# Kernel optimization log

Hardware: AMD Instinct MI355X
Metric: run time of the kernel (lower is better)

Reference implementation:

```python
import jax, jax.numpy as jnp
import numpy as np

B, SQ, SKV, DIN = 2, 2048, 2048, 2048
Q_HEADS, KV_HEADS, DIMS = 16, 4, 2048
HEAD_DIM = DIMS // Q_HEADS  # 128
REP = Q_HEADS // KV_HEADS   # 4


def setup_inputs() -> dict:
    key = jax.random.key(0)
    ks = jax.random.split(key, 6)
    scale = lambda fan_in: 1.0 / np.sqrt(fan_in)
    return {
        "q": jax.random.normal(ks[0], (B, SQ, DIN), jnp.float32),
        "kv": jax.random.normal(ks[1], (B, SKV, DIN), jnp.float32),
        "mask": jnp.ones((1, 1, SQ, SKV), jnp.float32),
        "Wq": jax.random.normal(ks[2], (DIN, Q_HEADS * HEAD_DIM), jnp.float32) * scale(DIN),
        "Wk": jax.random.normal(ks[3], (DIN, KV_HEADS * HEAD_DIM), jnp.float32) * scale(DIN),
        "Wv": jax.random.normal(ks[4], (DIN, KV_HEADS * HEAD_DIM), jnp.float32) * scale(DIN),
        "Wo": jax.random.normal(ks[5], (Q_HEADS * HEAD_DIM, DIN), jnp.float32) * scale(Q_HEADS * HEAD_DIM),
    }


def reference(q, kv, mask, Wq, Wk, Wv, Wo):
    b, sq, _ = q.shape
    skv = kv.shape[1]
    xq = q @ Wq                      # [b, sq, q_heads*head_dim]
    xk = kv @ Wk                     # [b, skv, kv_heads*head_dim]
    xv = kv @ Wv
    # faithful to source: element-wise repeat along feature axis, THEN head reshape
    xk = jnp.repeat(xk, REP, axis=-1)
    xv = jnp.repeat(xv, REP, axis=-1)
    xq = xq.reshape(b, sq, Q_HEADS, HEAD_DIM).transpose(0, 2, 1, 3)   # [b,h,sq,d]
    xk = xk.reshape(b, skv, Q_HEADS, HEAD_DIM).transpose(0, 2, 1, 3)  # [b,h,skv,d]
    xv = xv.reshape(b, skv, Q_HEADS, HEAD_DIM).transpose(0, 2, 1, 3)
    scores = jnp.einsum("bhqd,bhkd->bhqk", xq, xk) * (HEAD_DIM ** -0.5)
    scores = scores - (1.0 / mask - 1.0)
    attn = jax.nn.softmax(scores, axis=-1)
    out = jnp.einsum("bhqk,bhkd->bhqd", attn, xv)
    out = out.transpose(0, 2, 1, 3).reshape(b, sq, Q_HEADS * HEAD_DIM)
    return out @ Wo
```

## Files before the change

### kernel.cpp

```cpp
#include <hip/hip_runtime.h>
#include <hip/hip_bf16.h>
#include <stdint.h>

typedef short short8 __attribute__((ext_vector_type(8)));
typedef short short4v __attribute__((ext_vector_type(4)));
typedef float floatx4 __attribute__((ext_vector_type(4)));

#define AS1 __attribute__((address_space(1)))
#define AS3 __attribute__((address_space(3)))
#define DEV static __device__ __forceinline__

#if __has_builtin(__builtin_amdgcn_mfma_f32_16x16x16bf16_1k)
#define HAVE_MFMA16 1
#else
#define HAVE_MFMA16 0
#endif

DEV uint16_t f2bf(float x) {
  union { float f; uint32_t u; } v; v.f = x;
  return (uint16_t)((v.u + 0x7fffu + ((v.u >> 16) & 1u)) >> 16);
}

DEV uint32_t cvtpk(float a, float b) {
  uint32_t r;
  asm("v_cvt_pk_bf16_f32 %0, %1, %2" : "=v"(r) : "v"(a), "v"(b));
  return r;
}


DEV void cvt_bf16_f(const float* __restrict__ src, uint16_t* __restrict__ dst, int bid) {
  int i = bid * 256 + threadIdx.x;
  float4 v = ((const float4*)src)[i];
  union { uint16_t u[4]; uint64_t q; } o;
  o.u[0] = f2bf(v.x); o.u[1] = f2bf(v.y); o.u[2] = f2bf(v.z); o.u[3] = f2bf(v.w);
  ((uint64_t*)dst)[i] = o.q;
}

DEV void mask_scan_f(const float* __restrict__ mask, uint32_t* __restrict__ f, int bid) {
  int i = bid * 256 + threadIdx.x;
  const float4* p = (const float4*)mask;
  float4 a = p[i * 2], b = p[i * 2 + 1];
  bool bad = (a.x != 1.f) | (a.y != 1.f) | (a.z != 1.f) | (a.w != 1.f) |
             (b.x != 1.f) | (b.y != 1.f) | (b.z != 1.f) | (b.w != 1.f);
  if (bad) *f = 0u;
}

DEV void fold_wq_f(float (*tile)[33], const float* __restrict__ Wq,
                   uint16_t* __restrict__ WqFT, int bid) {
  const int t = threadIdx.x;
  const int j0 = (bid / 64) * 32, k0 = (bid % 64) * 32;
  {
    const int tj = t & 31, tk8 = t >> 5;
    const int j = j0 + tj;
    const int base = 128 * (j >> 5) + 4 * (j & 31);
    for (int kk = 0; kk < 4; ++kk) {
      int kl = tk8 * 4 + kk;
      float4 w = *(const float4*)(Wq + (size_t)(k0 + kl) * 2048 + base);
      tile[tj][kl] = w.x + w.y + w.z + w.w;
    }
  }
  __syncthreads();
  {
    const int tk = t & 31, tj8 = t >> 5;
    for (int jj = 0; jj < 4; ++jj) {
      int jl = tj8 * 4 + jj;
      WqFT[(size_t)(j0 + jl) * 2048 + k0 + tk] = f2bf(tile[jl][tk]);
    }
  }
}

DEV void wkv_t_f(float (*tile)[33], const float* __restrict__ Wk,
                 const float* __restrict__ Wv, uint16_t* __restrict__ WkvT, int bid) {
  const int t = threadIdx.x;
  const int j0 = (bid / 64) * 32, k0 = (bid % 64) * 32;
  const float* src = (j0 < 512) ? Wk : Wv;
  const int jb = (j0 < 512) ? j0 : j0 - 512;
  {
    const int tj = t & 31, tk8 = t >> 5;
    for (int kk = 0; kk < 4; ++kk) {
      int kl = tk8 * 4 + kk;
      tile[tj][kl] = src[(size_t)(k0 + kl) * 512 + jb + tj];
    }
  }
  __syncthreads();
  {
    const int tk = t & 31, tj8 = t >> 5;
    for (int jj = 0; jj < 4; ++jj) {
      int jl = tj8 * 4 + jj;
      WkvT[(size_t)(j0 + jl) * 2048 + k0 + tk] = f2bf(tile[jl][tk]);
    }
  }
}

DEV void wof_t_f(float (*tile)[33], const float* __restrict__ Wo,
                 uint16_t* __restrict__ WoFT, int bid) {
  const int t = threadIdx.x;
  const int n0 = (bid / 16) * 32, j0 = (bid % 16) * 32;
  {
    const int tn = t & 31, tj8 = t >> 5;
    for (int jj = 0; jj < 4; ++jj) {
      int jl = tj8 * 4 + jj;
      int j = j0 + jl;
      int base = 128 * (j >> 5) + 4 * (j & 31);
      float ssum = 0.f;
      for (int r = 0; r < 4; ++r) ssum += Wo[(size_t)(base + r) * 2048 + n0 + tn];
      tile[tn][jl] = ssum;
    }
  }
  __syncthreads();
  {
    const int tj = t & 31, tn8 = t >> 5;
    for (int nn = 0; nn < 4; ++nn) {
      int nl = tn8 * 4 + nn;
      WoFT[(size_t)(n0 + nl) * 512 + j0 + tj] = f2bf(tile[nl][tj]);
    }
  }
}

__global__ __launch_bounds__(256) void prep_k(const float* __restrict__ q,
                                              const float* __restrict__ kv,
                                              const float* __restrict__ mask,
                                              const float* __restrict__ Wq,
                                              const float* __restrict__ Wk,
                                              const float* __restrict__ Wv,
                                              const float* __restrict__ Wo,
                                              uint16_t* __restrict__ qb,
                                              uint16_t* __restrict__ kvb,
                                              uint16_t* __restrict__ WqFT,
                                              uint16_t* __restrict__ WkvT,
                                              uint16_t* __restrict__ WoFT,
                                              uint32_t* __restrict__ flag) {
  __shared__ float tile[32][33];
  const int bid = blockIdx.x;
  if (bid < 8192)        cvt_bf16_f(q, qb, bid);
  else if (bid < 16384)  cvt_bf16_f(kv, kvb, bid - 8192);
  else if (bid < 18432)  mask_scan_f(mask, flag, bid - 16384);
  else if (bid < 19456)  fold_wq_f(tile, Wq, WqFT, bid - 18432);
  else if (bid < 21504)  wkv_t_f(tile, Wk, Wv, WkvT, bid - 19456);
  else                   wof_t_f(tile, Wo, WoFT, bid - 21504);
}

template <typename OutT, int BM, int BN, int FA, int FB>
DEV void gemm_dev(uint16_t* __restrict__ As, uint16_t* __restrict__ Bs,
                  const uint16_t* __restrict__ A, const uint16_t* __restrict__ BT,
                  OutT* __restrict__ C, int N, int K, float scale, int m0, int n0) {
  constexpr int BK = 64;
  const int lane = threadIdx.x & 63, wave = threadIdx.x >> 6;
  const int lo = lane & 15, g = lane >> 4;
  const int wm = wave >> 1, wn = wave & 1;
  constexpr int CA = BM / 32, CB = BN / 32;
  floatx4 acc[FA][FB] = {};

  for (int k0 = 0; k0 < K; k0 += BK) {
#pragma unroll
    for (int c = 0; c < CA; ++c) {
      int slot = (wave * CA + c) * 64 + lane;
      int row = slot >> 3, col = (slot & 7) * 8;
      __builtin_amdgcn_global_load_lds((const AS1 uint32_t*)(A + (size_t)(m0 + row) * K + k0 + col),
                                       (AS3 uint32_t*)(As + (size_t)(wave * CA + c) * 512), 16, 0, 0);
    }
#pragma unroll
    for (int c = 0; c < CB; ++c) {
      int slot = (wave * CB + c) * 64 + lane;
      int row = slot >> 3, col = (slot & 7) * 8;
      __builtin_amdgcn_global_load_lds((const AS1 uint32_t*)(BT + (size_t)(n0 + row) * K + k0 + col),
                                       (AS3 uint32_t*)(Bs + (size_t)(wave * CB + c) * 512), 16, 0, 0);
    }
    __syncthreads();
#pragma unroll
    for (int kk = 0; kk < BK; kk += 32) {
      short8 af[FA], bf[FB];
#pragma unroll
      for (int fa = 0; fa < FA; ++fa)
        af[fa] = *(const short8*)&As[(wm * FA * 16 + fa * 16 + lo) * BK + kk + g * 8];
#pragma unroll
      for (int fb = 0; fb < FB; ++fb)
        bf[fb] = *(const short8*)&Bs[(wn * FB * 16 + fb * 16 + lo) * BK + kk + g * 8];
#pragma unroll
      for (int fa = 0; fa < FA; ++fa)
#pragma unroll
        for (int fb = 0; fb < FB; ++fb)
          acc[fa][fb] = __builtin_amdgcn_mfma_f32_16x16x32_bf16(af[fa], bf[fb], acc[fa][fb], 0, 0, 0);
    }
    __syncthreads();
  }
#pragma unroll
  for (int fa = 0; fa < FA; ++fa)
#pragma unroll
    for (int fb = 0; fb < FB; ++fb)
#pragma unroll
      for (int r = 0; r < 4; ++r) {
        int row = m0 + wm * FA * 16 + fa * 16 + g * 4 + r;
        int col = n0 + wn * FB * 16 + fb * 16 + lo;
        if constexpr (sizeof(OutT) == 2)
          C[(size_t)row * N + col] = (OutT)f2bf(acc[fa][fb][r] * scale);
        else
          C[(size_t)row * N + col] = (OutT)(acc[fa][fb][r] * scale);
      }
}

__global__ __launch_bounds__(256) void proj_k(const uint16_t* __restrict__ qb,
                                              const uint16_t* __restrict__ kvb,
                                              const uint16_t* __restrict__ WqFT,
                                              const uint16_t* __restrict__ WkvT,
                                              uint16_t* __restrict__ Qf,
                                              uint16_t* __restrict__ XK,
                                              uint16_t* __restrict__ VT,
                                              float scale2) {
  __shared__ __attribute__((aligned(16))) uint16_t As[128 * 64];
  __shared__ __attribute__((aligned(16))) uint16_t Bs[64 * 64];
  const int bid = blockIdx.x;
  const int lb = (bid & 7) * 96 + (bid >> 3);
  if (lb < 256) {
    gemm_dev<uint16_t, 128, 64, 4, 2>(As, Bs, qb, WqFT, Qf, 512, 2048, scale2,
                                      (lb >> 3) * 128, (lb & 7) * 64);
  } else if (lb < 512) {
    const int t = lb - 256;
    gemm_dev<uint16_t, 128, 64, 4, 2>(As, Bs, kvb, WkvT, XK, 512, 2048, 1.0f,
                                      (t >> 3) * 128, (t & 7) * 64);
  } else {
    const int t = lb - 512;
    const int b = t >> 7, r = t & 127;
    gemm_dev<uint16_t, 128, 64, 4, 2>(As, Bs, WkvT + 512 * 2048,
                                      kvb + (size_t)b * 2048 * 2048,
                                      VT + (size_t)b * 512 * 2048,
                                      2048, 2048, 1.0f, (r & 3) * 128, (r >> 2) * 64);
  }
}

__global__ __launch_bounds__(256) void oproj_k(const uint16_t* __restrict__ A,
                                               const uint16_t* __restrict__ BT,
                                               float* __restrict__ C) {
  __shared__ __attribute__((aligned(16))) uint16_t As[128 * 64];
  __shared__ __attribute__((aligned(16))) uint16_t Bs[64 * 64];
  const int lb = (blockIdx.x & 7) * 128 + (blockIdx.x >> 3);
  gemm_dev<float, 128, 64, 4, 2>(As, Bs, A, BT, C, 2048, 512, 1.0f,
                                 (lb >> 5) * 128, (lb & 31) * 64);
}

__global__ __launch_bounds__(256) void attn_k(const uint16_t* __restrict__ Qf,
                                              const uint16_t* __restrict__ XK,
                                              const uint16_t* __restrict__ VT,
                                              const float* __restrict__ mask,
                                              const uint32_t* __restrict__ flag,
                                              float* __restrict__ Pacc,
                                              float2* __restrict__ Pms) {
  __shared__ __attribute__((aligned(16))) uint16_t Ks[2][64 * 32];
  __shared__ __attribute__((aligned(16))) uint16_t Vs[2][32 * 64];
  const int tid = threadIdx.x;
  const int lane = tid & 63, w = tid >> 6;
  const int lo = lane & 15, g = lane >> 4;
  const int bid = blockIdx.x;
  const int lb = (bid & 7) * 256 + (bid >> 3);
  const int qt = lb & 31, h = (lb >> 5) & 15, b = (lb >> 9) & 1, half = lb >> 10;
  const int q0 = qt * 64 + w * 16;
  const int kvbase = half * 1024;
  const bool trivial = (*flag != 0u);
  const float LOG2E = 1.4426950408889634f;

  short8 qf = *(const short8*)(Qf + ((size_t)(b * 2048 + q0 + lo)) * 512 + h * 32 + g * 8);

  const int sK = w * 64 + lane;
  const int rK = sK >> 2;
  const int cKg = (sK & 3) ^ (rK & 3) ^ ((rK >> 2) & 3);
  const uint16_t* Ksrc = XK + ((size_t)(b * 2048 + kvbase + rK)) * 512 + h * 32 + cKg * 8;
  const int fV = sK >> 3, cV = ((sK & 7) - fV) & 7;
  const uint16_t* Vsrc = VT + ((size_t)(b * 512 + h * 32 + fV)) * 2048 + kvbase + cV * 8;

  const int swzL = (lo & 3) ^ ((lo >> 2) & 3);
  const int cK = (g ^ swzL) * 8;
#if !HAVE_MFMA16
  const int vA = (((g) + lo) & 7) * 8;
  const int vB = (((g + 4) + lo) & 7) * 8;
  const int srcA = lo + 16 * ((2 * g) & 3);
  const int srcB = lo + 16 * ((2 * g + 1) & 3);
#endif

  float m = -1e30f, sp = 0.f;
  floatx4 acc0 = {0.f, 0.f, 0.f, 0.f}, acc1 = {0.f, 0.f, 0.f, 0.f};
  const floatx4 zf = {0.f, 0.f, 0.f, 0.f};

  __builtin_amdgcn_global_load_lds((const AS1 uint32_t*)Ksrc,
                                   (AS3 uint32_t*)(&Ks[0][0] + w * 512), 16, 0, 0);
  __builtin_amdgcn_global_load_lds((const AS1 uint32_t*)Vsrc,
                                   (AS3 uint32_t*)(&Vs[0][0] + w * 512), 16, 0, 0);
  asm volatile("s_waitcnt vmcnt(0)" ::: "memory");
  __syncthreads();

  int buf = 0;
  for (int t = 0; t < 16; ++t) {
    if (t < 15) {
      __builtin_amdgcn_global_load_lds((const AS1 uint32_t*)(Ksrc + (size_t)(t + 1) * 64 * 512),
                                       (AS3 uint32_t*)(&Ks[buf ^ 1][0] + w * 512), 16, 0, 0);
      __builtin_amdgcn_global_load_lds((const AS1 uint32_t*)(Vsrc + (size_t)(t + 1) * 64),
                                       (AS3 uint32_t*)(&Vs[buf ^ 1][0] + w * 512), 16, 0, 0);
    }
    const uint16_t* Kb = &Ks[buf][0];
    const uint16_t* Vb = &Vs[buf][0];
    const int k0 = kvbase + t * 64;

    short8 kf0 = *(const short8*)(Kb + (lo) * 32 + cK);
    short8 kf1 = *(const short8*)(Kb + (lo + 16) * 32 + cK);
    short8 kf2 = *(const short8*)(Kb + (lo + 32) * 32 + cK);
    short8 kf3 = *(const short8*)(Kb + (lo + 48) * 32 + cK);
    floatx4 s0 = __builtin_amdgcn_mfma_f32_16x16x32_bf16(kf0, qf, zf, 0, 0, 0);
    floatx4 s1 = __builtin_amdgcn_mfma_f32_16x16x32_bf16(kf1, qf, zf, 0, 0, 0);
    floatx4 s2 = __builtin_amdgcn_mfma_f32_16x16x32_bf16(kf2, qf, zf, 0, 0, 0);
    floatx4 s3 = __builtin_amdgcn_mfma_f32_16x16x32_bf16(kf3, qf, zf, 0, 0, 0);

    if (!trivial) {
      const float* mp = mask + (size_t)(q0 + lo) * 2048 + k0 + g * 4;
      float4 m0v = *(const float4*)(mp);
      float4 m1v = *(const float4*)(mp + 16);
      float4 m2v = *(const float4*)(mp + 32);
      float4 m3v = *(const float4*)(mp + 48);
      s0[0] -= (1.f / m0v.x - 1.f) * LOG2E; s0[1] -= (1.f / m0v.y - 1.f) * LOG2E;
      s0[2] -= (1.f / m0v.z - 1.f) * LOG2E; s0[3] -= (1.f / m0v.w - 1.f) * LOG2E;
      s1[0] -= (1.f / m1v.x - 1.f) * LOG2E; s1[1] -= (1.f / m1v.y - 1.f) * LOG2E;
      s1[2] -= (1.f / m1v.z - 1.f) * LOG2E; s1[3] -= (1.f / m1v.w - 1.f) * LOG2E;
      s2[0] -= (1.f / m2v.x - 1.f) * LOG2E; s2[1] -= (1.f / m2v.y - 1.f) * LOG2E;
      s2[2] -= (1.f / m2v.z - 1.f) * LOG2E; s2[3] -= (1.f / m2v.w - 1.f) * LOG2E;
      s3[0] -= (1.f / m3v.x - 1.f) * LOG2E; s3[1] -= (1.f / m3v.y - 1.f) * LOG2E;
      s3[2] -= (1.f / m3v.z - 1.f) * LOG2E; s3[3] -= (1.f / m3v.w - 1.f) * LOG2E;
    }

    float t0 = fmaxf(fmaxf(s0[0], s0[1]), s0[2]);
    float t1 = fmaxf(fmaxf(s0[3], s1[0]), s1[1]);
    float t2 = fmaxf(fmaxf(s1[2], s1[3]), s2[0]);
    float t3 = fmaxf(fmaxf(s2[1], s2[2]), s2[3]);
    float t4 = fmaxf(fmaxf(s3[0], s3[1]), s3[2]);
    float pmax = fmaxf(fmaxf(fmaxf(t0, t1), t2), fmaxf(fmaxf(t3, t4), s3[3]));

    if (!__all(pmax - m <= 8.f)) {
      float tm = fmaxf(pmax, __shfl_xor(pmax, 16));
      tm = fmaxf(tm, __shfl_xor(tm, 32));
      float mn = fmaxf(m, tm);
      float f = __builtin_amdgcn_exp2f(m - mn);
      sp *= f;
#pragma unroll
      for (int r = 0; r < 4; ++r) { acc0[r] *= f; acc1[r] *= f; }
      m = mn;
    }

    float p0[4], p1[4], p2[4], p3[4];
#pragma unroll
    for (int r = 0; r < 4; ++r) {
      p0[r] = __builtin_amdgcn_exp2f(s0[r] - m);
      p1[r] = __builtin_amdgcn_exp2f(s1[r] - m);
      p2[r] = __builtin_amdgcn_exp2f(s2[r] - m);
      p3[r] = __builtin_amdgcn_exp2f(s3[r] - m);
    }
    sp += ((p0[0] + p0[1]) + (p0[2] + p0[3])) + ((p1[0] + p1[1]) + (p1[2] + p1[3])) +
          ((p2[0] + p2[1]) + (p2[2] + p2[3])) + ((p3[0] + p3[1]) + (p3[2] + p3[3]));

#if HAVE_MFMA16
#pragma unroll
    for (int c = 0; c < 4; ++c) {
      const float* pc = (c == 0) ? p0 : (c == 1) ? p1 : (c == 2) ? p2 : p3;
      union { uint32_t u[2]; short4v v; } pk;
      pk.u[0] = cvtpk(pc[0], pc[1]);
      pk.u[1] = cvtpk(pc[2], pc[3]);
      const int kc = 2 * c + (g >> 1);
      const int pA = (kc + lo) & 7;
      const int pB = (kc + lo + 16) & 7;
      short4v va = *(const short4v*)(Vb + lo * 64 + pA * 8 + (g & 1) * 4);
      short4v vb = *(const short4v*)(Vb + (lo + 16) * 64 + pB * 8 + (g & 1) * 4);
      acc0 = __builtin_amdgcn_mfma_f32_16x16x16bf16_1k(va, pk.v, acc0, 0, 0, 0);
      acc1 = __builtin_amdgcn_mfma_f32_16x16x16bf16_1k(vb, pk.v, acc1, 0, 0, 0);
    }
#else
    uint32_t u0 = cvtpk(p0[0], p0[1]), u1 = cvtpk(p0[2], p0[3]);
    uint32_t u2 = cvtpk(p1[0], p1[1]), u3 = cvtpk(p1[2], p1[3]);
    uint32_t u4 = cvtpk(p2[0], p2[1]), u5 = cvtpk(p2[2], p2[3]);
    uint32_t u6 = cvtpk(p3[0], p3[1]), u7 = cvtpk(p3[2], p3[3]);
    union { uint32_t u[4]; short8 v; } pfa, pfb;
    {
      uint32_t x0 = (uint32_t)__shfl((int)u0, srcA), x2 = (uint32_t)__shfl((int)u2, srcA);
      uint32_t x1 = (uint32_t)__shfl((int)u1, srcA), x3 = (uint32_t)__shfl((int)u3, srcA);
      uint32_t y0 = (uint32_t)__shfl((int)u0, srcB), y2 = (uint32_t)__shfl((int)u2, srcB);
      uint32_t y1 = (uint32_t)__shfl((int)u1, srcB), y3 = (uint32_t)__shfl((int)u3, srcB);
      pfa.u[0] = (g < 2) ? x0 : x2;
      pfa.u[1] = (g < 2) ? x1 : x3;
      pfa.u[2] = (g < 2) ? y0 : y2;
      pfa.u[3] = (g < 2) ? y1 : y3;
    }
    {
      uint32_t x4 = (uint32_t)__shfl((int)u4, srcA), x6 = (uint32_t)__shfl((int)u6, srcA);
      uint32_t x5 = (uint32_t)__shfl((int)u5, srcA), x7 = (uint32_t)__shfl((int)u7, srcA);
      uint32_t y4 = (uint32_t)__shfl((int)u4, srcB), y6 = (uint32_t)__shfl((int)u6, srcB);
      uint32_t y5 = (uint32_t)__shfl((int)u5, srcB), y7 = (uint32_t)__shfl((int)u7, srcB);
      pfb.u[0] = (g < 2) ? x4 : x6;
      pfb.u[1] = (g < 2) ? x5 : x7;
      pfb.u[2] = (g < 2) ? y4 : y6;
      pfb.u[3] = (g < 2) ? y5 : y7;
    }
    short8 v0a = *(const short8*)(Vb + lo * 64 + vA);
    short8 v1a = *(const short8*)(Vb + (lo + 16) * 64 + vA);
    short8 v0b = *(const short8*)(Vb + lo * 64 + vB);
    short8 v1b = *(const short8*)(Vb + (lo + 16) * 64 + vB);
    acc0 = __builtin_amdgcn_mfma_f32_16x16x32_bf16(v0a, pfa.v, acc0, 0, 0, 0);
    acc1 = __builtin_amdgcn_mfma_f32_16x16x32_bf16(v1a, pfa.v, acc1, 0, 0, 0);
    acc0 = __builtin_amdgcn_mfma_f32_16x16x32_bf16(v0b, pfb.v, acc0, 0, 0, 0);
    acc1 = __builtin_amdgcn_mfma_f32_16x16x32_bf16(v1b, pfb.v, acc1, 0, 0, 0);
#endif

    asm volatile("s_waitcnt vmcnt(0)" ::: "memory");
    __syncthreads();
    buf ^= 1;
  }
  float s = sp;
  s += __shfl_xor(s, 16);
  s += __shfl_xor(s, 32);

  const size_t qidx = ((size_t)((half * 2 + b) * 16 + h)) * 2048 + q0 + lo;
  float* pacc = Pacc + qidx * 32;
  *(floatx4*)(pacc + 4 * g) = acc0;
  *(floatx4*)(pacc + 16 + 4 * g) = acc1;
  if (g == 0) Pms[qidx] = make_float2(m, s);
}

__global__ __launch_bounds__(256) void combine_k(const float* __restrict__ Pacc,
                                                 const float2* __restrict__ Pms,
                                                 uint16_t* __restrict__ O32) {
  const int t = blockIdx.x * 256 + threadIdx.x;
  const int f4 = t & 7;
  const int qq = (t >> 3) & 2047;
  const int h = (t >> 14) & 15;
  const int b = t >> 18;
  const size_t qidx0 = ((size_t)((0 + b) * 16 + h)) * 2048 + qq;
  const size_t qidx1 = ((size_t)((2 + b) * 16 + h)) * 2048 + qq;
  float2 ms0 = Pms[qidx0], ms1 = Pms[qidx1];
  float M = fmaxf(ms0.x, ms1.x);
  float w0 = __builtin_amdgcn_exp2f(ms0.x - M);
  float w1 = __builtin_amdgcn_exp2f(ms1.x - M);
  float inv = 1.0f / (ms0.y * w0 + ms1.y * w1);
  w0 *= inv; w1 *= inv;
  float4 a0 = *(const float4*)(Pacc + qidx0 * 32 + f4 * 4);
  float4 a1 = *(const float4*)(Pacc + qidx1 * 32 + f4 * 4);
  union { uint16_t u[4]; uint64_t q; } o;
  o.u[0] = f2bf(a0.x * w0 + a1.x * w1);
  o.u[1] = f2bf(a0.y * w0 + a1.y * w1);
  o.u[2] = f2bf(a0.z * w0 + a1.z * w1);
  o.u[3] = f2bf(a0.w * w0 + a1.w * w1);
  *(uint64_t*)(O32 + ((size_t)(b * 2048 + qq)) * 512 + h * 32 + f4 * 4) = o.q;
}

extern "C" void kernel_launch(void* const* d_in, const int* in_sizes, int n_in,
                              void* d_out, int out_size, void* d_ws, size_t ws_size,
                              hipStream_t stream) {
  const float* q    = (const float*)d_in[0];
  const float* kv   = (const float*)d_in[1];
  const float* mask = (const float*)d_in[2];
  const float* Wq   = (const float*)d_in[3];
  const float* Wk   = (const float*)d_in[4];
  const float* Wv   = (const float*)d_in[5];
  const float* Wo   = (const float*)d_in[6];

  char* ws = (char*)d_ws;
  uint16_t* qb    = (uint16_t*)(ws);
  uint16_t* kvb   = (uint16_t*)(ws + (16ull << 20));
  uint16_t* Qf    = (uint16_t*)(ws + (32ull << 20));
  uint16_t* XK    = (uint16_t*)(ws + (36ull << 20));
  uint16_t* VT    = (uint16_t*)(ws + (40ull << 20));
  uint16_t* O32   = (uint16_t*)(ws + (48ull << 20));
  uint16_t* WqFT  = (uint16_t*)(ws + (52ull << 20));
  uint16_t* WkvT  = (uint16_t*)(ws + (54ull << 20));
  uint16_t* WoFT  = (uint16_t*)(ws + (58ull << 20));
  uint32_t* flag  = (uint32_t*)(ws + (60ull << 20));
  float*    Pacc  = (float*)(ws);
  float2*   Pms   = (float2*)(ws + (16ull << 20));

  const float SCALE2 = 0.08838834764831845f * 1.4426950408889634f;

  hipMemsetAsync(flag, 1, 4, stream);
  prep_k<<<22528, 256, 0, stream>>>(q, kv, mask, Wq, Wk, Wv, Wo,
                                    qb, kvb, WqFT, WkvT, WoFT, flag);
  proj_k<<<768, 256, 0, stream>>>(qb, kvb, WqFT, WkvT, Qf, XK, VT, SCALE2);
  attn_k<<<2048, 256, 0, stream>>>(Qf, XK, VT, mask, flag, Pacc, Pms);
  combine_k<<<2048, 256, 0, stream>>>(Pacc, Pms, O32);
  oproj_k<<<1024, 256, 0, stream>>>(O32, WoFT, (float*)d_out);
}
```

Before: 141.4 us.

## Double-buffer LDS tiles in GEMM to overlap global loads with MFMA

The shared GEMM routine now keeps two LDS buffers for A and B and issues the next K-tile's global-to-LDS loads before computing on the current tile. Each iteration then ends with one vmcnt wait and barrier instead of two barriers, so load latency can hide behind MFMA work in the projection and output-projection kernels. In exchange, LDS use per block doubles to 48 KB, which may lower occupancy.

```diff
diff --git a/kernel.cpp b/kernel.cpp
--- a/kernel.cpp
+++ b/kernel.cpp
@@ -151,38 +151,54 @@
   constexpr int CA = BM / 32, CB = BN / 32;
   floatx4 acc[FA][FB] = {};
 
-  for (int k0 = 0; k0 < K; k0 += BK) {
+  auto stage = [&](int bf, int kk0) {
 #pragma unroll
     for (int c = 0; c < CA; ++c) {
       int slot = (wave * CA + c) * 64 + lane;
       int row = slot >> 3, col = (slot & 7) * 8;
-      __builtin_amdgcn_global_load_lds((const AS1 uint32_t*)(A + (size_t)(m0 + row) * K + k0 + col),
-                                       (AS3 uint32_t*)(As + (size_t)(wave * CA + c) * 512), 16, 0, 0);
+      __builtin_amdgcn_global_load_lds(
+          (const AS1 uint32_t*)(A + (size_t)(m0 + row) * K + kk0 + col),
+          (AS3 uint32_t*)(As + (size_t)bf * BM * BK + (size_t)(wave * CA + c) * 512),
+          16, 0, 0);
     }
 #pragma unroll
     for (int c = 0; c < CB; ++c) {
       int slot = (wave * CB + c) * 64 + lane;
       int row = slot >> 3, col = (slot & 7) * 8;
-      __builtin_amdgcn_global_load_lds((const AS1 uint32_t*)(BT + (size_t)(n0 + row) * K + k0 + col),
-                                       (AS3 uint32_t*)(Bs + (size_t)(wave * CB + c) * 512), 16, 0, 0);
-    }
+      __builtin_amdgcn_global_load_lds(
+          (const AS1 uint32_t*)(BT + (size_t)(n0 + row) * K + kk0 + col),
+          (AS3 uint32_t*)(Bs + (size_t)bf * BN * BK + (size_t)(wave * CB + c) * 512),
+          16, 0, 0);
+    }
+  };
+
+  stage(0, 0);
+  asm volatile("s_waitcnt vmcnt(0)" ::: "memory");
+  __syncthreads();
+
+  int bf = 0;
+  for (int k0 = 0; k0 < K; k0 += BK) {
+    if (k0 + BK < K) stage(bf ^ 1, k0 + BK);
+    const uint16_t* Ab = As + (size_t)bf * BM * BK;
+    const uint16_t* Bb = Bs + (size_t)bf * BN * BK;
+#pragma unroll
+    for (int kk = 0; kk < BK; kk += 32) {
+      short8 af[FA], bfr[FB];
+#pragma unroll
+      for (int fa = 0; fa < FA; ++fa)
+        af[fa] = *(const short8*)&Ab[(wm * FA * 16 + fa * 16 + lo) * BK + kk + g * 8];
+#pragma unroll
+      for (int fb = 0; fb < FB; ++fb)
+        bfr[fb] = *(const short8*)&Bb[(wn * FB * 16 + fb * 16 + lo) * BK + kk + g * 8];
+#pragma unroll
+      for (int fa = 0; fa < FA; ++fa)
+#pragma unroll
+        for (int fb = 0; fb < FB; ++fb)
+          acc[fa][fb] = __builtin_amdgcn_mfma_f32_16x16x32_bf16(af[fa], bfr[fb], acc[fa][fb], 0, 0, 0);
+    }
+    asm volatile("s_waitcnt vmcnt(0)" ::: "memory");
     __syncthreads();
-#pragma unroll
-    for (int kk = 0; kk < BK; kk += 32) {
-      short8 af[FA], bf[FB];
-#pragma unroll
-      for (int fa = 0; fa < FA; ++fa)
-        af[fa] = *(const short8*)&As[(wm * FA * 16 + fa * 16 + lo) * BK + kk + g * 8];
-#pragma unroll
-      for (int fb = 0; fb < FB; ++fb)
-        bf[fb] = *(const short8*)&Bs[(wn * FB * 16 + fb * 16 + lo) * BK + kk + g * 8];
-#pragma unroll
-      for (int fa = 0; fa < FA; ++fa)
-#pragma unroll
-        for (int fb = 0; fb < FB; ++fb)
-          acc[fa][fb] = __builtin_amdgcn_mfma_f32_16x16x32_bf16(af[fa], bf[fb], acc[fa][fb], 0, 0, 0);
-    }
-    __syncthreads();
+    bf ^= 1;
   }
 #pragma unroll
   for (int fa = 0; fa < FA; ++fa)
@@ -207,8 +223,8 @@
                                               uint16_t* __restrict__ XK,
                                               uint16_t* __restrict__ VT,
                                               float scale2) {
-  __shared__ __attribute__((aligned(16))) uint16_t As[128 * 64];
-  __shared__ __attribute__((aligned(16))) uint16_t Bs[64 * 64];
+  __shared__ __attribute__((aligned(16))) uint16_t As[2 * 128 * 64];
+  __shared__ __attribute__((aligned(16))) uint16_t Bs[2 * 64 * 64];
   const int bid = blockIdx.x;
   const int lb = (bid & 7) * 96 + (bid >> 3);
   if (lb < 256) {
@@ -231,8 +247,8 @@
 __global__ __launch_bounds__(256) void oproj_k(const uint16_t* __restrict__ A,
                                                const uint16_t* __restrict__ BT,
                                                float* __restrict__ C) {
-  __shared__ __attribute__((aligned(16))) uint16_t As[128 * 64];
-  __shared__ __attribute__((aligned(16))) uint16_t Bs[64 * 64];
+  __shared__ __attribute__((aligned(16))) uint16_t As[2 * 128 * 64];
+  __shared__ __attribute__((aligned(16))) uint16_t Bs[2 * 64 * 64];
   const int lb = (blockIdx.x & 7) * 128 + (blockIdx.x >> 3);
   gemm_dev<float, 128, 64, 4, 2>(As, Bs, A, BT, C, 2048, 512, 1.0f,
                                  (lb >> 5) * 128, (lb & 31) * 64);
```

New measurement: 151.0 us. 6.8% more time.
